# Optimization experiments

Measured on AMD Instinct MI355X. Metric: run time of the kernel, lower is better.

Reference implementation:

```python
import jax, jax.numpy as jnp
import numpy as np

E = 512
H = 8
SL = (16, 16, 16)
B = 4
LEN = np.array([768, 640, 704, 600], dtype=np.int32)


def _starts(lengths):
    cs = jnp.cumsum(lengths)
    starts = jnp.concatenate([jnp.zeros((1,), cs.dtype), cs[:-1]])
    return starts, cs


def _tile_within(data, lengths, buffer):
    # per-token causal window [cur, cur-1, ..., cur-L]; slots before sample start come from buffer
    L = buffer.shape[0]
    N = data.shape[0]
    starts, cs = _starts(lengths)
    g = jnp.arange(N)
    sid = jnp.searchsorted(cs, g, side='right')
    qpos = g - starts[sid]
    src = qpos[:, None] - jnp.arange(L + 1)[None, :]  # [N, L+1]
    from_data = src >= 0
    didx = jnp.clip(starts[sid][:, None] + src, 0, N - 1)
    bidx = jnp.clip(L + src, 0, L - 1)
    return jnp.where(from_data[:, :, None], data[didx], buffer[bidx])


def _mlp(h, w1, b1, w2, b2):
    return jax.nn.gelu(h @ w1 + b1, approximate=False) @ w2 + b2


def _selection(eu, lengths, win):
    # faithful port of the no_grad selection block (B > 1 branch)
    N = eu.shape[0]
    starts, _ = _starts(lengths)
    ends = starts + lengths - 1
    running = jnp.cumsum(eu)
    end_u = running[ends]
    sample_u = jnp.concatenate([end_u[:1], end_u[2:] - end_u[1:-1]])
    running = running - jnp.cumsum(jnp.zeros((N,), eu.dtype).at[starts[1:]].set(sample_u))
    offs = jnp.cumsum(jnp.zeros((N,), eu.dtype).at[starts[1:]].set(lengths[:-1].astype(eu.dtype)))
    idxs = jnp.arange(1, N + 1, dtype=eu.dtype) - offs
    selected = (eu > running / idxs) | (idxs <= win)
    csel = jnp.cumsum(selected.astype(jnp.int32))
    end_counts = csel[ends]
    next_lengths = jnp.concatenate([end_counts[:1], end_counts[1:] - end_counts[:-1]])
    take_map = csel - csel[0]  # unique_consecutive inverse of a 0/1-increment cumsum
    return jnp.nonzero(selected)[0], next_lengths, take_map


def _forward(args, lengths, sels):
    (x, kv_w, kv_b, q_w, q_b, proj_w, proj_b, buf0, buf1, buf2,
     d0_w1, d0_b1, d0_w2, d0_b2, d1_w1, d1_b1, d1_w2, d1_b2,
     u0_w1, u0_b1, u0_w2, u0_b2, u1_w1, u1_b1, u1_w2, u1_b2,
     wq, bq, wk, bk, wv, bv, out_w, out_b) = args
    Ls = [int(v) for v in np.asarray(lengths)]
    x_flat = jnp.concatenate([x[b, :Ls[b]] for b in range(len(Ls))])  # [N0, E]
    kv0 = x_flat @ kv_w + kv_b  # [N0, 2E]
    # scale 0
    tiled0 = _tile_within(kv0, lengths, buf0)  # [N0, SL0, 2E]
    eu0 = jax.nn.elu(_mlp(tiled0.reshape(tiled0.shape[0], -1), u0_w1, u0_b1, u0_w2, u0_b2))[:, 0] + 1.0
    s0 = _selection(jax.lax.stop_gradient(eu0), lengths, SL[0]) if sels is None else sels[0]
    sel0, len1, tm0 = s0
    selt0 = jnp.take(tiled0, sel0, 0)
    r0 = jax.nn.softmax(_mlp(selt0.reshape(selt0.shape[0], -1), d0_w1, d0_b1, d0_w2, d0_b2), -1)
    dat1 = jnp.sum(selt0 * r0[:, :, None], -2)  # [N1, 2E]
    util0 = _tile_within(jnp.take(eu0, sel0, 0)[:, None], len1, jnp.zeros((SL[1] - 1, 1), eu0.dtype))
    # scale 1
    tiled1 = _tile_within(dat1, len1, buf1)  # [N1, SL1, 2E]
    eu1 = jax.nn.elu(_mlp(tiled1.reshape(tiled1.shape[0], -1), u1_w1, u1_b1, u1_w2, u1_b2))[:, 0] + 1.0
    s1 = _selection(jax.lax.stop_gradient(eu1), len1, SL[1]) if sels is None else sels[1]
    sel1, len2, tm1 = s1
    selt1 = jnp.take(tiled1, sel1, 0)
    r1 = jax.nn.softmax(_mlp(selt1.reshape(selt1.shape[0], -1), d1_w1, d1_b1, d1_w2, d1_b2), -1)
    dat2 = jnp.sum(selt1 * r1[:, :, None], -2)  # [N2, 2E]
    util1 = _tile_within(jnp.take(eu1, sel1, 0)[:, None], len2, jnp.zeros((SL[2] - 1, 1), eu1.dtype))
    tiled2 = _tile_within(dat2, len2, buf2)  # [N2, SL2, 2E]
    # per-token multi-scale kv context (reconstructed tail of truncated forward)
    idx1 = tm0
    idx2 = jnp.take(tm1, idx1)
    win1 = jnp.take(tiled1, idx1, 0) * jnp.take(util0, idx1, 0)
    win2 = jnp.take(tiled2, idx2, 0) * jnp.take(util1, idx2, 0)
    kv = jnp.concatenate([tiled0, win1, win2], 1)  # [N0, sum(SL), 2E]
    k = kv[..., :E]
    v = kv[..., E:]
    q = x_flat @ q_w + q_b
    N0 = q.shape[0]
    Skv = kv.shape[1]
    hd = E // H
    qh = (q @ wq + bq).reshape(N0, H, hd)
    kh = (k @ wk + bk).reshape(N0, Skv, H, hd)
    vh = (v @ wv + bv).reshape(N0, Skv, H, hd)
    attn = jax.nn.softmax(jnp.einsum('nhd,nshd->nhs', qh, kh) / float(np.sqrt(hd)), -1)
    ctx = jnp.einsum('nhs,nshd->nhd', attn, vh).reshape(N0, E)
    y = (ctx @ out_w + out_b) @ proj_w + proj_b  # dropout in eval mode == identity
    out = jnp.zeros((len(Ls), max(Ls), E), y.dtype)
    off = 0
    for b, Lb in enumerate(Ls):
        out = out.at[b, :Lb].set(y[off:off + Lb])
        off += Lb
    return out, (s0, s1)


def setup_inputs():
    ks = list(jax.random.split(jax.random.key(0), 64))
    it = iter(ks)

    def nrm(shape, s=0.02):
        return jax.random.normal(next(it), shape, jnp.float32) * s

    def uni(shape):
        return jax.random.uniform(next(it), shape, dtype=jnp.float32)

    F = 2 * E
    inp = {
        'x': jax.random.normal(next(it), (B, int(LEN.max()), E), jnp.float32),
        'lengths': jnp.array(LEN),
        'kv_w': nrm((E, F)), 'kv_b': jnp.zeros((F,), jnp.float32),
        'q_w': nrm((E, E)), 'q_b': jnp.zeros((E,), jnp.float32),
        'proj_w': nrm((E, E)), 'proj_b': jnp.zeros((E,), jnp.float32),
        'buf0': uni((SL[0] - 1, F)), 'buf1': uni((SL[1] - 1, F)), 'buf2': uni((SL[2] - 1, F)),
    }
    for li in (0, 1):
        sl = SL[li]
        din, hid = sl * F, sl * 10
        inp['d%d_w1' % li] = nrm((din, hid)); inp['d%d_b1' % li] = jnp.zeros((hid,), jnp.float32)
        inp['d%d_w2' % li] = nrm((hid, sl)); inp['d%d_b2' % li] = jnp.zeros((sl,), jnp.float32)
        inp['u%d_w1' % li] = nrm((din, hid)); inp['u%d_b1' % li] = jnp.zeros((hid,), jnp.float32)
        inp['u%d_w2' % li] = nrm((hid, 1)); inp['u%d_b2' % li] = jnp.zeros((1,), jnp.float32)
    inp.update({'wq': nrm((E, E)), 'bq': jnp.zeros((E,), jnp.float32),
                'wk': nrm((E, E)), 'bk': jnp.zeros((E,), jnp.float32),
                'wv': nrm((E, E)), 'bv': jnp.zeros((E,), jnp.float32),
                'out_w': nrm((E, E)), 'out_b': jnp.zeros((E,), jnp.float32)})
    return inp


def reference(x, lengths, kv_w, kv_b, q_w, q_b, proj_w, proj_b, buf0, buf1, buf2,
              d0_w1, d0_b1, d0_w2, d0_b2, d1_w1, d1_b1, d1_w2, d1_b2,
              u0_w1, u0_b1, u0_w2, u0_b2, u1_w1, u1_b1, u1_w2, u1_b2,
              wq, bq, wk, bk, wv, bv, out_w, out_b):
    args = (x, kv_w, kv_b, q_w, q_b, proj_w, proj_b, buf0, buf1, buf2,
            d0_w1, d0_b1, d0_w2, d0_b2, d1_w1, d1_b1, d1_w2, d1_b2,
            u0_w1, u0_b1, u0_w2, u0_b2, u1_w1, u1_b1, u1_w2, u1_b2,
            wq, bq, wk, bk, wv, bv, out_w, out_b)
    out, _ = _forward(args, lengths, None)
    return out
```

## Files before the change

### kernel.cpp

```cpp
#include <hip/hip_runtime.h>
#include <cstddef>

#define DEVFN __device__ __forceinline__

constexpr int N0   = 2712;
constexpr int MAXL = 768;
constexpr int NBAT = 4;
constexpr int E    = 512;
constexpr int F    = 1024;
constexpr int HID  = 160;
constexpr int WSZ  = 16;
constexpr int NY   = 2 * WSZ * HID;
constexpr int XSTR = 7680;
constexpr int YC0  = 2560;
constexpr size_t NOFF = (size_t)-1;

constexpr size_t oXF    = 0;
constexpr size_t oXO    = oXF    + (size_t)N0*E;
constexpr size_t oEU0   = oXO    + (size_t)N0*XSTR;
constexpr size_t oDAT1  = oEU0   + (size_t)N0;
constexpr size_t oEU1   = oDAT1  + (size_t)N0*F;
constexpr size_t oDAT2  = oEU1   + (size_t)N0;
constexpr size_t oBH0K  = oDAT2  + (size_t)N0*F;
constexpr size_t oBH0V  = oBH0K  + (size_t)15*E;
constexpr size_t oDH1K  = oBH0V  + (size_t)15*E;
constexpr size_t oDH1V  = oDH1K  + (size_t)N0*E;
constexpr size_t oDH2K  = oDH1V  + (size_t)N0*E;
constexpr size_t oDH2V  = oDH2K  + (size_t)N0*E;
constexpr size_t oCTX   = oDH2V  + (size_t)N0*E;
constexpr size_t oY2    = oCTX   + (size_t)N0*E;
constexpr size_t oEUS0  = oY2    + (size_t)N0*E;
constexpr size_t oEUS1  = oEUS0  + (size_t)N0;
constexpr size_t oSEL0  = oEUS1  + (size_t)N0;
constexpr size_t oTM0   = oSEL0  + (size_t)N0;
constexpr size_t oSEL1  = oTM0   + (size_t)N0;
constexpr size_t oTM1   = oSEL1  + (size_t)N0;
constexpr size_t oB0    = oTM1   + (size_t)N0;
constexpr size_t oB1    = oB0    + 8;
constexpr size_t oB2    = oB1    + 8;
constexpr size_t oWOP   = oB2    + 8;
constexpr size_t oBOP   = oWOP   + (size_t)E*E;
constexpr size_t oWX    = oBOP   + E;
constexpr size_t oXB    = oWX    + (size_t)E*XSTR;
constexpr size_t oBD0   = oXB    + XSTR;
constexpr size_t oBD1   = oBD0   + (size_t)F*NY;
constexpr size_t oBUFY0 = oBD1   + (size_t)F*NY;
constexpr size_t oBUFY1 = oBUFY0 + (size_t)15*NY;
constexpr size_t oYB    = oBUFY1 + (size_t)15*NY;
constexpr size_t oEND   = oYB    + (size_t)N0*NY;

__device__ float g_pool[oEND];

DEVFN float geluf(float x) {
    return 0.5f * x * (1.0f + erff(x / 1.41421356237309504880f));
}

__global__ void k_init() {
    if (threadIdx.x == 0) {
        int* b = (int*)(g_pool + oB0);
        b[0] = 0; b[1] = 768; b[2] = 1408; b[3] = 2112; b[4] = N0;
    }
}

__global__ __launch_bounds__(256) void k_xflat(const float* __restrict__ x) {
    int idx = blockIdx.x * 256 + threadIdx.x;
    if (idx >= N0 * E) return;
    int d = idx & (E - 1);
    int g = idx >> 9;
    int s = (g >= 768) + (g >= 1408) + (g >= 2112);
    const int st[4] = {0, 768, 1408, 2112};
    int qp = g - st[s];
    g_pool[oXF + idx] = x[((size_t)s * MAXL + qp) * E + d];
}

__global__ __launch_bounds__(256) void k_reshape(
    const float* __restrict__ uw, const float* __restrict__ dw, size_t bdOff)
{
    int idx = blockIdx.x * 256 + threadIdx.x;
    if (idx >= F * NY) return;
    int col = idx % NY;
    int f = idx / NY;
    const float* src = (col < NY / 2) ? uw : dw;
    int rem = (col < NY / 2) ? col : col - NY / 2;
    int j = rem / HID, n = rem % HID;
    g_pool[bdOff + idx] = src[((size_t)j * F + f) * HID + n];
}

__global__ __launch_bounds__(256) void k_copymat(
    const float* __restrict__ src, size_t dstOff, int rows, int cols, int lds, int ldd)
{
    int idx = blockIdx.x * 256 + threadIdx.x;
    if (idx >= rows * cols) return;
    int r = idx / cols, c = idx % cols;
    g_pool[dstOff + (size_t)r * ldd + c] = src[(size_t)r * lds + c];
}

__global__ __launch_bounds__(256) void k_prepvec(
    const float* __restrict__ kv_b, const float* __restrict__ q_b, const float* __restrict__ out_b,
    const float* __restrict__ wk, const float* __restrict__ bk,
    const float* __restrict__ wv, const float* __restrict__ bv,
    const float* __restrict__ wq, const float* __restrict__ bq,
    const float* __restrict__ proj_w, const float* __restrict__ proj_b)
{
    int idx = blockIdx.x * 256 + threadIdx.x;
    if (idx >= 3072) return;
    if (idx < 1024) { g_pool[oXB + idx] = kv_b[idx]; return; }
    const float* vec; const float* W; const float* add; int n; size_t dst;
    if (idx < 1536)      { n = idx - 1024; vec = kv_b;     W = wk;     add = bk;     dst = oXB + idx; }
    else if (idx < 2048) { n = idx - 1536; vec = kv_b + E; W = wv;     add = bv;     dst = oXB + idx; }
    else if (idx < 2560) { n = idx - 2048; vec = q_b;      W = wq;     add = bq;     dst = oXB + idx; }
    else                 { n = idx - 2560; vec = out_b;    W = proj_w; add = proj_b; dst = oBOP + n; }
    float s = add[n];
    for (int k = 0; k < E; ++k) s = fmaf(vec[k], W[(size_t)k * E + n], s);
    g_pool[dst] = s;
}

__global__ __launch_bounds__(256) void k_cvec(const float* __restrict__ kv_b) {
    int n = blockIdx.x * 256 + threadIdx.x;
    if (n >= NY) return;
    const float* BD = g_pool + oBD0;
    float s = 0.0f;
    for (int k = 0; k < F; ++k) s = fmaf(kv_b[k], BD[(size_t)k * NY + n], s);
    g_pool[oXB + YC0 + n] = s;
}

DEVFN void gemm64_body(
    const float* __restrict__ A, int lda,
    const float* __restrict__ B, int ldb,
    const float* __restrict__ bias,
    float* __restrict__ C, int ldc,
    int mval, int row0, int col0, int K, int N)
{
    __shared__ __align__(16) float As[32][68];
    __shared__ __align__(16) float Bs[32][64];

    int tid = threadIdx.x;
    float acc[4][4] = {};
    int tx = tid & 15, ty = tid >> 4;

    for (int k0 = 0; k0 < K; k0 += 32) {
        #pragma unroll
        for (int l = 0; l < 8; ++l) {
            int idx = tid + l * 256;
            int kk = idx & 31, m = idx >> 5;
            int r = row0 + m;
            float v = 0.0f;
            if (r < mval) v = A[(size_t)r * lda + k0 + kk];
            As[kk][m] = v;
        }
        #pragma unroll
        for (int l = 0; l < 8; ++l) {
            int idx = tid + l * 256;
            int n = idx & 63, kk = idx >> 6;
            int col = col0 + n;
            float v = 0.0f;
            if (col < N) v = B[(size_t)(k0 + kk) * ldb + col];
            Bs[kk][n] = v;
        }
        __syncthreads();
        #pragma unroll
        for (int kk = 0; kk < 32; ++kk) {
            float4 a4 = *(const float4*)&As[kk][ty * 4];
            float4 b4 = *(const float4*)&Bs[kk][tx * 4];
            float av[4] = {a4.x, a4.y, a4.z, a4.w};
            float bv[4] = {b4.x, b4.y, b4.z, b4.w};
            #pragma unroll
            for (int i = 0; i < 4; ++i)
                #pragma unroll
                for (int jn = 0; jn < 4; ++jn)
                    acc[i][jn] = fmaf(av[i], bv[jn], acc[i][jn]);
        }
        __syncthreads();
    }

    #pragma unroll
    for (int i = 0; i < 4; ++i) {
        int r = row0 + ty * 4 + i;
        if (r >= mval) continue;
        #pragma unroll
        for (int jn = 0; jn < 4; ++jn) {
            int col = col0 + tx * 4 + jn;
            if (col < N)
                C[(size_t)r * ldc + col] = acc[i][jn] + (bias ? bias[col] : 0.0f);
        }
    }
}

__global__ __launch_bounds__(256) void k_pgemm(
    size_t Aoff, int lda, size_t Boff, int ldb, size_t biasOff,
    size_t Coff, int ldc, int M, size_t mdevOff, int K, int N)
{
    int mval = (mdevOff == NOFF) ? M : *(const int*)(g_pool + mdevOff);
    int row0 = blockIdx.x * 64, col0 = blockIdx.y * 64;
    if (row0 >= mval) return;
    gemm64_body(g_pool + Aoff, lda, g_pool + Boff, ldb,
                (biasOff == NOFF) ? nullptr : g_pool + biasOff,
                g_pool + Coff, ldc, mval, row0, col0, K, N);
}

__global__ __launch_bounds__(256) void k_wprep(
    const float* __restrict__ kv_w, const float* __restrict__ q_w, const float* __restrict__ out_w,
    const float* __restrict__ wk, const float* __restrict__ wv,
    const float* __restrict__ wq, const float* __restrict__ proj_w)
{
    int z = blockIdx.z;
    const float* A; int lda; const float* B; float* C; int ldc;
    if (z == 0)      { A = kv_w;     lda = F; B = wk;     C = g_pool + oWX + 1024; ldc = XSTR; }
    else if (z == 1) { A = kv_w + E; lda = F; B = wv;     C = g_pool + oWX + 1536; ldc = XSTR; }
    else if (z == 2) { A = q_w;      lda = E; B = wq;     C = g_pool + oWX + 2048; ldc = XSTR; }
    else             { A = out_w;    lda = E; B = proj_w; C = g_pool + oWOP;       ldc = E;    }
    gemm64_body(A, lda, B, E, nullptr, C, ldc, E, blockIdx.x * 64, blockIdx.y * 64, E, E);
}

__global__ __launch_bounds__(256) void k_bufy(
    const float* __restrict__ buf0, const float* __restrict__ buf1)
{
    int z = blockIdx.z;
    const float* A = z ? buf1 : buf0;
    const float* B = g_pool + (z ? oBD1 : oBD0);
    float* C = g_pool + (z ? oBUFY1 : oBUFY0);
    gemm64_body(A, F, B, NY, nullptr, C, NY, 15, 0, blockIdx.y * 64, F, NY);
}

__global__ __launch_bounds__(256) void k_bh(
    const float* __restrict__ buf0,
    const float* __restrict__ wk, const float* __restrict__ bk,
    const float* __restrict__ wv, const float* __restrict__ bv)
{
    int z = blockIdx.z;
    const float* A = buf0 + (size_t)z * E;
    const float* B = z ? wv : wk;
    const float* bias = z ? bv : bk;
    float* C = g_pool + (z ? oBH0V : oBH0K);
    gemm64_body(A, F, B, E, bias, C, E, 15, 0, blockIdx.y * 64, E, E);
}

DEVFN void fma_8x8(const float4& a0, const float4& a1, const float4& b0, const float4& b1,
                   float2 (&acc)[8][4])
{
    float av[8] = {a0.x, a0.y, a0.z, a0.w, a1.x, a1.y, a1.z, a1.w};
    float2 bv[4] = {make_float2(b0.x, b0.y), make_float2(b0.z, b0.w),
                    make_float2(b1.x, b1.y), make_float2(b1.z, b1.w)};
    #pragma unroll
    for (int i = 0; i < 8; ++i) {
        #pragma unroll
        for (int q = 0; q < 4; ++q) {
            acc[i][q].x = fmaf(av[i], bv[q].x, acc[i][q].x);
            acc[i][q].y = fmaf(av[i], bv[q].y, acc[i][q].y);
        }
    }
}

DEVFN void gemm128_body(
    const float* __restrict__ A, int lda,
    const float* __restrict__ B, int ldb,
    const float* __restrict__ bias,
    float* __restrict__ C, int ldc,
    int mval, int row0, int col0, int K)
{
    __shared__ __align__(16) float As[16][132];
    __shared__ __align__(16) float Bs[16][132];

    int tid = threadIdx.x;
    int tx = tid & 15, ty = tid >> 4;
    float2 acc[8][4] = {};

    int ar = tid >> 1, akq = (tid & 1) * 8;
    int bk = tid >> 4, bnq = (tid & 15) * 8;

    for (int k0 = 0; k0 < K; k0 += 16) {
        {
            float4 v0 = make_float4(0.f, 0.f, 0.f, 0.f), v1 = v0;
            int rr = row0 + ar;
            if (rr < mval) {
                v0 = *(const float4*)&A[(size_t)rr * lda + k0 + akq];
                v1 = *(const float4*)&A[(size_t)rr * lda + k0 + akq + 4];
            }
            As[akq + 0][ar] = v0.x; As[akq + 1][ar] = v0.y;
            As[akq + 2][ar] = v0.z; As[akq + 3][ar] = v0.w;
            As[akq + 4][ar] = v1.x; As[akq + 5][ar] = v1.y;
            As[akq + 6][ar] = v1.z; As[akq + 7][ar] = v1.w;
        }
        {
            const float* bp = &B[(size_t)(k0 + bk) * ldb + col0 + bnq];
            *(float4*)&Bs[bk][bnq]     = *(const float4*)&bp[0];
            *(float4*)&Bs[bk][bnq + 4] = *(const float4*)&bp[4];
        }
        __syncthreads();

        float4 a0A = *(const float4*)&As[0][ty * 8];
        float4 a1A = *(const float4*)&As[0][ty * 8 + 4];
        float4 b0A = *(const float4*)&Bs[0][tx * 4];
        float4 b1A = *(const float4*)&Bs[0][64 + tx * 4];
        #pragma unroll
        for (int kk = 0; kk < 16; kk += 2) {
            float4 a0B = *(const float4*)&As[kk + 1][ty * 8];
            float4 a1B = *(const float4*)&As[kk + 1][ty * 8 + 4];
            float4 b0B = *(const float4*)&Bs[kk + 1][tx * 4];
            float4 b1B = *(const float4*)&Bs[kk + 1][64 + tx * 4];
            fma_8x8(a0A, a1A, b0A, b1A, acc);
            if (kk + 2 < 16) {
                a0A = *(const float4*)&As[kk + 2][ty * 8];
                a1A = *(const float4*)&As[kk + 2][ty * 8 + 4];
                b0A = *(const float4*)&Bs[kk + 2][tx * 4];
                b1A = *(const float4*)&Bs[kk + 2][64 + tx * 4];
            }
            fma_8x8(a0B, a1B, b0B, b1B, acc);
        }
        __syncthreads();
    }

    #pragma unroll
    for (int i = 0; i < 8; ++i) {
        int r = row0 + ty * 8 + i;
        if (r >= mval) continue;
        float o0[4], o1[4];
        o0[0] = acc[i][0].x; o0[1] = acc[i][0].y; o0[2] = acc[i][1].x; o0[3] = acc[i][1].y;
        o1[0] = acc[i][2].x; o1[1] = acc[i][2].y; o1[2] = acc[i][3].x; o1[3] = acc[i][3].y;
        if (bias) {
            #pragma unroll
            for (int jn = 0; jn < 4; ++jn) {
                o0[jn] += bias[col0 + tx * 4 + jn];
                o1[jn] += bias[col0 + 64 + tx * 4 + jn];
            }
        }
        *(float4*)&C[(size_t)r * ldc + col0 + tx * 4]      = *(float4*)&o0[0];
        *(float4*)&C[(size_t)r * ldc + col0 + 64 + tx * 4] = *(float4*)&o1[0];
    }
}

__global__ __launch_bounds__(256) void k_tgemm(
    size_t Aoff, int lda, size_t Boff, int ldb, size_t biasOff,
    size_t Coff, int ldc, int M, size_t mdevOff, int K)
{
    int mval = (mdevOff == NOFF) ? M : *(const int*)(g_pool + mdevOff);
    int row0 = blockIdx.x * 128, col0 = blockIdx.y * 128;
    if (row0 >= mval) return;
    gemm128_body(g_pool + Aoff, lda, g_pool + Boff, ldb,
                 (biasOff == NOFF) ? nullptr : g_pool + biasOff,
                 g_pool + Coff, ldc, mval, row0, col0, K);
}

__global__ __launch_bounds__(256) void k_wy(const float* __restrict__ kv_w) {
    int z = blockIdx.z;
    const float* A = kv_w + z * 256;
    const float* B = g_pool + oBD0 + (size_t)z * 256 * NY;
    float* C = g_pool + oYB + (size_t)z * E * NY;
    gemm128_body(A, F, B, NY, nullptr, C, NY, E, blockIdx.x * 128, blockIdx.y * 128, 256);
}

__global__ __launch_bounds__(256) void k_wyred() {
    int idx = blockIdx.x * 256 + threadIdx.x;
    if (idx >= E * NY) return;
    int r = idx / NY, c = idx % NY;
    const float* p = g_pool + oYB;
    float s = ((p[idx] + p[(size_t)E * NY + idx]) + p[(size_t)2 * E * NY + idx]) + p[(size_t)3 * E * NY + idx];
    g_pool[oWX + (size_t)r * XSTR + YC0 + c] = s;
}

__global__ __launch_bounds__(256) void k_zgemm(
    const float* __restrict__ wk, const float* __restrict__ wv)
{
    int z = blockIdx.z;
    int mval = *(const int*)(g_pool + ((z < 2) ? (oB1 + 4) : (oB2 + 4)));
    int row0 = blockIdx.x * 64, col0 = blockIdx.y * 64;
    if (row0 >= mval) return;
    const float* A = g_pool + ((z < 2) ? oDAT1 : oDAT2) + (size_t)(z & 1) * E;
    const float* B = (z & 1) ? wv : wk;
    float* C = g_pool + oDH1K + (size_t)z * N0 * E;
    gemm64_body(A, F, B, E, nullptr, C, E, mval, row0, col0, E, E);
}

__global__ void k_huev(
    size_t boundsOff, size_t yOff, int yStr, size_t bufYOff,
    const float* __restrict__ b1, const float* __restrict__ w2, const float* __restrict__ b2,
    size_t euOff, size_t mdevOff, int M)
{
    int i = blockIdx.x;
    int mval = (mdevOff == NOFF) ? M : *(const int*)(g_pool + mdevOff);
    if (i >= mval) return;
    int n = threadIdx.x;

    __shared__ float t[HID];
    const int* bounds = (const int*)(g_pool + boundsOff);
    int b1i = bounds[1], b2i = bounds[2], b3i = bounds[3];
    int s = (i >= b1i) + (i >= b2i) + (i >= b3i);
    int st = (s == 0) ? 0 : ((s == 1) ? b1i : ((s == 2) ? b2i : b3i));
    int qp = i - st;

    const float* Y = g_pool + yOff;
    const float* bufY = g_pool + bufYOff;

    if (n < HID) {
        float acc = b1[n];
        #pragma unroll
        for (int j = 0; j < WSZ; ++j) {
            int sp = qp - j;
            const float* row = (sp >= 0) ? &Y[(size_t)(i - j) * yStr]
                                         : &bufY[(size_t)(15 + sp) * NY];
            acc += row[j * HID + n];
        }
        t[n] = geluf(acc) * w2[n];
    }
    __syncthreads();
    if (n == 0) {
        float v = b2[0];
        for (int k = 0; k < HID; ++k) v += t[k];
        v = (v > 0.0f) ? v : expm1f(v);
        g_pool[euOff + i] = v + 1.0f;
    }
}

__global__ __launch_bounds__(256) void k_select(
    size_t euOff, size_t boundsOff, int win,
    size_t selOff, size_t tmOff, size_t euSelOff, size_t boundsNextOff)
{
    __shared__ __align__(16) float se[N0];
    __shared__ __align__(16) float run[N0];
    __shared__ int sFlag[N0];
    __shared__ int sSum[256];
    __shared__ float sCz[NBAT];
    __shared__ int sEc[NBAT];
    __shared__ int sB[5];

    int tid = threadIdx.x;
    const int* bounds = (const int*)(g_pool + boundsOff);
    if (tid < 5) sB[tid] = bounds[tid];
    __syncthreads();
    int N = sB[4];
    for (int i = tid; i < N; i += 256) se[i] = g_pool[euOff + i];
    __syncthreads();

    if (tid == 0) {
        float r = 0.0f;
        int g = 0;
        for (; g + 8 <= N; g += 8) {
            float4 a = *(const float4*)&se[g];
            float4 b4 = *(const float4*)&se[g + 4];
            r += a.x;  run[g]     = r;
            r += a.y;  run[g + 1] = r;
            r += a.z;  run[g + 2] = r;
            r += a.w;  run[g + 3] = r;
            r += b4.x; run[g + 4] = r;
            r += b4.y; run[g + 5] = r;
            r += b4.z; run[g + 6] = r;
            r += b4.w; run[g + 7] = r;
        }
        for (; g < N; ++g) { r += se[g]; run[g] = r; }
        float e0 = run[sB[1] - 1], e1 = run[sB[2] - 1], e2 = run[sB[3] - 1];
        float su0 = e0;
        float su1 = e2 - e1;
        float su2 = run[sB[4] - 1] - e2;
        sCz[0] = 0.0f;
        sCz[1] = su0;
        sCz[2] = su0 + su1;
        sCz[3] = (su0 + su1) + su2;
    }
    __syncthreads();

    for (int g = tid; g < N; g += 256) {
        int seg = (g >= sB[1]) + (g >= sB[2]) + (g >= sB[3]);
        int st = (seg == 0) ? 0 : sB[seg];
        int qp1 = g - st + 1;
        float r2 = run[g] - sCz[seg];
        bool seld = (se[g] > r2 / (float)qp1) || (qp1 <= win);
        sFlag[g] = seld ? 1 : 0;
    }
    __syncthreads();

    int CH = (N + 255) >> 8;
    int lo = tid * CH, hi = min(lo + CH, N);
    {
        int s = 0;
        for (int g = lo; g < hi; ++g) s += sFlag[g];
        sSum[tid] = s;
    }
    __syncthreads();
    if (tid == 0) {
        int acc = 0;
        for (int t = 0; t < 256; ++t) { int v = sSum[t]; sSum[t] = acc; acc += v; }
    }
    __syncthreads();

    int* sel = (int*)(g_pool + selOff);
    int* tm  = (int*)(g_pool + tmOff);
    float* eus = g_pool + euSelOff;
    int* bn  = (int*)(g_pool + boundsNextOff);

    int csel0 = sFlag[0];
    {
        int csel = sSum[tid];
        for (int g = lo; g < hi; ++g) {
            csel += sFlag[g];
            tm[g] = csel - csel0;
            if (sFlag[g]) { sel[csel - 1] = g; eus[csel - 1] = se[g]; }
            #pragma unroll
            for (int s = 0; s < NBAT; ++s)
                if (g == sB[s + 1] - 1) sEc[s] = csel;
        }
    }
    __syncthreads();
    if (tid == 0) {
        bn[0] = 0; bn[1] = sEc[0]; bn[2] = sEc[1]; bn[3] = sEc[2]; bn[4] = sEc[3];
    }
}

__global__ __launch_bounds__(256) void k_rdat(
    size_t boundsOff, size_t yOff, int yStr, size_t bufYOff,
    const float* __restrict__ b1, const float* __restrict__ w2, const float* __restrict__ b2,
    size_t selOff, size_t mdevOff,
    size_t srcOff, int srcStr, const float* __restrict__ buf,
    size_t datOff)
{
    int i = blockIdx.x;
    if (i >= *(const int*)(g_pool + mdevOff)) return;
    const float* src = g_pool + srcOff;
    const int* bounds = (const int*)(g_pool + boundsOff);
    const int* sel = (const int*)(g_pool + selOff);
    float* dat = g_pool + datOff;

    __shared__ float gh[HID];
    __shared__ float sv[WSZ];
    __shared__ float r[WSZ];
    __shared__ int sG, sQp;

    int tid = threadIdx.x;
    if (tid == 0) {
        int g = sel[i];
        int b1i = bounds[1], b2i = bounds[2], b3i = bounds[3];
        int s = (g >= b1i) + (g >= b2i) + (g >= b3i);
        int st = (s == 0) ? 0 : ((s == 1) ? b1i : ((s == 2) ? b2i : b3i));
        sG = g; sQp = g - st;
    }
    __syncthreads();
    int g = sG, qp = sQp;

    if (tid < HID) {
        const float* Y = g_pool + yOff;
        const float* bufY = g_pool + bufYOff;
        float acc = b1[tid];
        #pragma unroll
        for (int j = 0; j < WSZ; ++j) {
            int sp = qp - j;
            const float* row = (sp >= 0) ? &Y[(size_t)(g - j) * yStr]
                                         : &bufY[(size_t)(15 + sp) * NY];
            acc += row[NY / 2 + j * HID + tid];
        }
        gh[tid] = geluf(acc);
    }
    __syncthreads();
    if (tid < WSZ) {
        float acc = 0.0f;
        for (int k = 0; k < HID; ++k) acc += gh[k] * w2[k * WSZ + tid];
        sv[tid] = acc + b2[tid];
    }
    __syncthreads();
    if (tid == 0) {
        float m = sv[0];
        for (int t = 1; t < WSZ; ++t) m = fmaxf(m, sv[t]);
        float sum = 0.0f;
        for (int t = 0; t < WSZ; ++t) { float e = expf(sv[t] - m); r[t] = e; sum += e; }
        for (int t = 0; t < WSZ; ++t) r[t] = r[t] / sum;
    }
    __syncthreads();
    for (int f = tid; f < F; f += 256) {
        float acc = 0.0f;
        for (int j = 0; j < WSZ; ++j) {
            int sp = qp - j;
            float v = (sp >= 0) ? src[(size_t)(g - j) * srcStr + f]
                                : buf[(size_t)(15 + sp) * F + f];
            acc = fmaf(r[j], v, acc);
        }
        dat[(size_t)i * F + f] = acc;
    }
}

__global__ __launch_bounds__(512) void k_attn(
    const float* __restrict__ bk, const float* __restrict__ bv)
{
    int g = blockIdx.x;
    const float* XO   = g_pool + oXO;
    const float* BH0k = g_pool + oBH0K;
    const float* BH0v = g_pool + oBH0V;
    const float* DH1k = g_pool + oDH1K;
    const float* DH1v = g_pool + oDH1V;
    const float* DH2k = g_pool + oDH2K;
    const float* DH2v = g_pool + oDH2V;
    const float* eus0 = g_pool + oEUS0;
    const float* eus1 = g_pool + oEUS1;
    const int* tm0 = (const int*)(g_pool + oTM0);
    const int* tm1 = (const int*)(g_pool + oTM1);
    const int* bounds1 = (const int*)(g_pool + oB1);
    const int* bounds2 = (const int*)(g_pool + oB2);

    __shared__ const float* sK[48];
    __shared__ const float* sV[48];
    __shared__ float sScale[48];
    __shared__ __align__(16) float sQ[E], sBk[E], sBv[E];
    __shared__ float sc[48][8];

    int tid = threadIdx.x;
    sQ[tid]  = XO[(size_t)g * XSTR + 2048 + tid];
    sBk[tid] = bk[tid];
    sBv[tid] = bv[tid];

    if (tid < 48) {
        int s = tid;
        const float *pK = nullptr, *pV = nullptr;
        float scl = 0.0f;
        if (s < 16) {
            int s0 = (g >= 768) + (g >= 1408) + (g >= 2112);
            const int st0[4] = {0, 768, 1408, 2112};
            int sp = (g - st0[s0]) - s;
            if (sp >= 0) { pK = XO + (size_t)(g - s) * XSTR + 1024; pV = XO + (size_t)(g - s) * XSTR + 1536; }
            else         { pK = BH0k + (size_t)(15 + sp) * E; pV = BH0v + (size_t)(15 + sp) * E; }
            scl = 1.0f;
        } else if (s < 32) {
            int j = s - 16;
            int i1 = tm0[g];
            int b1 = bounds1[1], b2 = bounds1[2], b3 = bounds1[3];
            int sg = (i1 >= b1) + (i1 >= b2) + (i1 >= b3);
            int st = (sg == 0) ? 0 : ((sg == 1) ? b1 : ((sg == 2) ? b2 : b3));
            int sp = (i1 - st) - j;
            if (sp >= 0) { pK = DH1k + (size_t)(i1 - j) * E; pV = DH1v + (size_t)(i1 - j) * E; scl = eus0[i1 - j]; }
        } else {
            int j = s - 32;
            int i1 = tm0[g];
            int i2 = tm1[i1];
            int b1 = bounds2[1], b2 = bounds2[2], b3 = bounds2[3];
            int sg = (i2 >= b1) + (i2 >= b2) + (i2 >= b3);
            int st = (sg == 0) ? 0 : ((sg == 1) ? b1 : ((sg == 2) ? b2 : b3));
            int sp = (i2 - st) - j;
            if (sp >= 0) { pK = DH2k + (size_t)(i2 - j) * E; pV = DH2v + (size_t)(i2 - j) * E; scl = eus1[i2 - j]; }
        }
        sK[s] = pK; sV[s] = pV; sScale[s] = scl;
    }
    __syncthreads();

    if (tid < 384) {
        int s = tid >> 3, h = tid & 7;
        const float* bp = sK[s];
        float scl = sScale[s];
        float acc = 0.0f;
        int d0 = h * 64;
        if (s < 16) {
            for (int d = 0; d < 64; d += 4) {
                float4 qv = *(const float4*)&sQ[d0 + d];
                float4 kv4 = *(const float4*)&bp[d0 + d];
                acc += qv.x * kv4.x; acc += qv.y * kv4.y;
                acc += qv.z * kv4.z; acc += qv.w * kv4.w;
            }
        } else if (bp) {
            for (int d = 0; d < 64; d += 4) {
                float4 qv = *(const float4*)&sQ[d0 + d];
                float4 kv4 = *(const float4*)&bp[d0 + d];
                float4 bb = *(const float4*)&sBk[d0 + d];
                acc += qv.x * (bb.x + scl * kv4.x); acc += qv.y * (bb.y + scl * kv4.y);
                acc += qv.z * (bb.z + scl * kv4.z); acc += qv.w * (bb.w + scl * kv4.w);
            }
        } else {
            for (int d = 0; d < 64; d += 4) {
                float4 qv = *(const float4*)&sQ[d0 + d];
                float4 bb = *(const float4*)&sBk[d0 + d];
                acc += qv.x * bb.x; acc += qv.y * bb.y;
                acc += qv.z * bb.z; acc += qv.w * bb.w;
            }
        }
        sc[s][h] = acc * 0.125f;
    }
    __syncthreads();

    if (tid < 8) {
        int h = tid;
        float m = sc[0][h];
        for (int s = 1; s < 48; ++s) m = fmaxf(m, sc[s][h]);
        float sum = 0.0f;
        for (int s = 0; s < 48; ++s) { float e = expf(sc[s][h] - m); sc[s][h] = e; sum += e; }
        for (int s = 0; s < 48; ++s) sc[s][h] = sc[s][h] / sum;
    }
    __syncthreads();

    {
        int d = tid, h = d >> 6;
        float acc = 0.0f;
        for (int s = 0; s < 48; ++s) {
            const float* bp = sV[s];
            float vv;
            if (s < 16) vv = bp[d];
            else        vv = sBv[d] + (bp ? sScale[s] * bp[d] : 0.0f);
            acc = fmaf(sc[s][h], vv, acc);
        }
        g_pool[oCTX + (size_t)g * E + d] = acc;
    }
}

__global__ __launch_bounds__(256) void k_scatter(float* __restrict__ out) {
    int idx = blockIdx.x * 256 + threadIdx.x;
    if (idx >= NBAT * MAXL * E) return;
    int d = idx & (E - 1);
    int rest = idx >> 9;
    int p = rest % MAXL, bb = rest / MAXL;
    const int st[4] = {0, 768, 1408, 2112};
    const int ln[4] = {768, 640, 704, 600};
    out[idx] = (p < ln[bb]) ? g_pool[oY2 + (size_t)(st[bb] + p) * E + d] : 0.0f;
}

extern "C" void kernel_launch(void* const* d_in, const int* in_sizes, int n_in,
                              void* d_out, int out_size, void* d_ws, size_t ws_size,
                              hipStream_t stream)
{
    (void)in_sizes; (void)n_in; (void)d_ws; (void)ws_size; (void)out_size;

    const float* x      = (const float*)d_in[0];
    const float* kv_w   = (const float*)d_in[2];
    const float* kv_b   = (const float*)d_in[3];
    const float* q_w    = (const float*)d_in[4];
    const float* q_b    = (const float*)d_in[5];
    const float* proj_w = (const float*)d_in[6];
    const float* proj_b = (const float*)d_in[7];
    const float* buf0   = (const float*)d_in[8];
    const float* buf1   = (const float*)d_in[9];
    const float* d0_w1  = (const float*)d_in[11];
    const float* d0_b1  = (const float*)d_in[12];
    const float* d0_w2  = (const float*)d_in[13];
    const float* d0_b2  = (const float*)d_in[14];
    const float* u0_w1  = (const float*)d_in[15];
    const float* u0_b1  = (const float*)d_in[16];
    const float* u0_w2  = (const float*)d_in[17];
    const float* u0_b2  = (const float*)d_in[18];
    const float* d1_w1  = (const float*)d_in[19];
    const float* d1_b1  = (const float*)d_in[20];
    const float* d1_w2  = (const float*)d_in[21];
    const float* d1_b2  = (const float*)d_in[22];
    const float* u1_w1  = (const float*)d_in[23];
    const float* u1_b1  = (const float*)d_in[24];
    const float* u1_w2  = (const float*)d_in[25];
    const float* u1_b2  = (const float*)d_in[26];
    const float* wq     = (const float*)d_in[27];
    const float* bq     = (const float*)d_in[28];
    const float* wk     = (const float*)d_in[29];
    const float* bk     = (const float*)d_in[30];
    const float* wv     = (const float*)d_in[31];
    const float* bv     = (const float*)d_in[32];
    const float* out_w  = (const float*)d_in[33];
    const float* out_b  = (const float*)d_in[34];

    auto cdiv = [](int a, int b) { return (a + b - 1) / b; };
    auto GT = [&](int M, int N) { return dim3(cdiv(M, 128), cdiv(N, 128)); };

    k_init<<<1, 64, 0, stream>>>();
    k_xflat<<<cdiv(N0 * E, 256), 256, 0, stream>>>(x);

    k_reshape<<<cdiv(F * NY, 256), 256, 0, stream>>>(u0_w1, d0_w1, oBD0);
    k_reshape<<<cdiv(F * NY, 256), 256, 0, stream>>>(u1_w1, d1_w1, oBD1);
    k_copymat<<<cdiv(E * F, 256), 256, 0, stream>>>(kv_w, oWX, E, F, F, XSTR);
    k_wprep<<<dim3(8, 8, 4), 256, 0, stream>>>(kv_w, q_w, out_w, wk, wv, wq, proj_w);
    k_prepvec<<<cdiv(3072, 256), 256, 0, stream>>>(kv_b, q_b, out_b, wk, bk, wv, bv, wq, bq, proj_w, proj_b);
    k_cvec<<<cdiv(NY, 256), 256, 0, stream>>>(kv_b);
    k_wy<<<dim3(4, 40, 4), 256, 0, stream>>>(kv_w);
    k_wyred<<<cdiv(E * NY, 256), 256, 0, stream>>>();
    k_bufy<<<dim3(1, NY / 64, 2), 256, 0, stream>>>(buf0, buf1);
    k_bh<<<dim3(1, E / 64, 2), 256, 0, stream>>>(buf0, wk, bk, wv, bv);

    k_tgemm<<<GT(N0, XSTR), 256, 0, stream>>>(oXF, E, oWX, XSTR, oXB, oXO, XSTR, N0, NOFF, E);

    k_huev<<<N0, 160, 0, stream>>>(oB0, oXO + YC0, XSTR, oBUFY0, u0_b1, u0_w2, u0_b2, oEU0, NOFF, N0);
    k_select<<<1, 256, 0, stream>>>(oEU0, oB0, WSZ, oSEL0, oTM0, oEUS0, oB1);
    k_rdat<<<N0, 256, 0, stream>>>(oB0, oXO + YC0, XSTR, oBUFY0, d0_b1, d0_w2, d0_b2, oSEL0, oB1 + 4, oXO, XSTR, buf0, oDAT1);

    k_tgemm<<<GT(N0, NY), 256, 0, stream>>>(oDAT1, F, oBD1, NY, NOFF, oYB, NY, N0, oB1 + 4, F);
    k_huev<<<N0, 160, 0, stream>>>(oB1, oYB, NY, oBUFY1, u1_b1, u1_w2, u1_b2, oEU1, oB1 + 4, N0);
    k_select<<<1, 256, 0, stream>>>(oEU1, oB1, WSZ, oSEL1, oTM1, oEUS1, oB2);
    k_rdat<<<N0, 256, 0, stream>>>(oB1, oYB, NY, oBUFY1, d1_b1, d1_w2, d1_b2, oSEL1, oB2 + 4, oDAT1, F, buf1, oDAT2);

    k_zgemm<<<dim3(cdiv(N0, 64), E / 64, 4), 256, 0, stream>>>(wk, wv);

    k_attn<<<N0, 512, 0, stream>>>(bk, bv);
    k_pgemm<<<dim3(cdiv(N0, 64), E / 64), 256, 0, stream>>>(oCTX, E, oWOP, E, oBOP, oY2, E, N0, NOFF, E, E);
    k_scatter<<<cdiv(NBAT * MAXL * E, 256), 256, 0, stream>>>((float*)d_out);
}
```

Measured before the change: 1.380 ms.

## Fold scale-1 K/V projections into the level-1 GEMM and vectorise rdat accumulation

Extends the level-1 weight matrix with block-diagonal wk/wv columns (zero-padded halves), so the scale-1 K/V projections come out of the existing DAT1 GEMM instead of a separate zgemm pass. The zgemm launch shrinks to the scale-2 K and V only, and attention reads scale-1 K/V directly from the widened YB buffer. Separately, k_rdat now has each thread accumulate four contiguous features with float4 loads. The fused GEMM multiplies against zero blocks, wasting about half its FLOPs on the new columns, and the assumption F==4*256 is baked into rdat.

```diff
diff --git a/kernel.cpp b/kernel.cpp
--- a/kernel.cpp
+++ b/kernel.cpp
@@ -11,6 +11,9 @@
 constexpr int HID  = 160;
 constexpr int WSZ  = 16;
 constexpr int NY   = 2 * WSZ * HID;
+constexpr int NY1  = 6144;
+constexpr int DH1KC = 5120;
+constexpr int DH1VC = 5632;
 constexpr int XSTR = 7680;
 constexpr int YC0  = 2560;
 constexpr size_t NOFF = (size_t)-1;
@@ -23,9 +26,7 @@
 constexpr size_t oDAT2  = oEU1   + (size_t)N0;
 constexpr size_t oBH0K  = oDAT2  + (size_t)N0*F;
 constexpr size_t oBH0V  = oBH0K  + (size_t)15*E;
-constexpr size_t oDH1K  = oBH0V  + (size_t)15*E;
-constexpr size_t oDH1V  = oDH1K  + (size_t)N0*E;
-constexpr size_t oDH2K  = oDH1V  + (size_t)N0*E;
+constexpr size_t oDH2K  = oBH0V  + (size_t)15*E;
 constexpr size_t oDH2V  = oDH2K  + (size_t)N0*E;
 constexpr size_t oCTX   = oDH2V  + (size_t)N0*E;
 constexpr size_t oY2    = oCTX   + (size_t)N0*E;
@@ -44,10 +45,10 @@
 constexpr size_t oXB    = oWX    + (size_t)E*XSTR;
 constexpr size_t oBD0   = oXB    + XSTR;
 constexpr size_t oBD1   = oBD0   + (size_t)F*NY;
-constexpr size_t oBUFY0 = oBD1   + (size_t)F*NY;
+constexpr size_t oBUFY0 = oBD1   + (size_t)F*NY1;
 constexpr size_t oBUFY1 = oBUFY0 + (size_t)15*NY;
 constexpr size_t oYB    = oBUFY1 + (size_t)15*NY;
-constexpr size_t oEND   = oYB    + (size_t)N0*NY;
+constexpr size_t oEND   = oYB    + (size_t)N0*NY1;
 
 __device__ float g_pool[oEND];
 
@@ -84,6 +85,30 @@
     int rem = (col < NY / 2) ? col : col - NY / 2;
     int j = rem / HID, n = rem % HID;
     g_pool[bdOff + idx] = src[((size_t)j * F + f) * HID + n];
+}
+
+__global__ __launch_bounds__(256) void k_bd1x(
+    const float* __restrict__ uw, const float* __restrict__ dw,
+    const float* __restrict__ wk, const float* __restrict__ wv)
+{
+    int idx = blockIdx.x * 256 + threadIdx.x;
+    if (idx >= F * NY1) return;
+    int col = idx % NY1;
+    int f = idx / NY1;
+    float v;
+    if (col < NY) {
+        const float* src = (col < NY / 2) ? uw : dw;
+        int rem = (col < NY / 2) ? col : col - NY / 2;
+        int j = rem / HID, n = rem % HID;
+        v = src[((size_t)j * F + f) * HID + n];
+    } else if (col < DH1VC) {
+        int m = col - DH1KC;
+        v = (f < E) ? wk[(size_t)f * E + m] : 0.0f;
+    } else {
+        int m = col - DH1VC;
+        v = (f >= E) ? wv[(size_t)(f - E) * E + m] : 0.0f;
+    }
+    g_pool[oBD1 + idx] = v;
 }
 
 __global__ __launch_bounds__(256) void k_copymat(
@@ -218,8 +243,9 @@
     int z = blockIdx.z;
     const float* A = z ? buf1 : buf0;
     const float* B = g_pool + (z ? oBD1 : oBD0);
+    int ldb = z ? NY1 : NY;
     float* C = g_pool + (z ? oBUFY1 : oBUFY0);
-    gemm64_body(A, F, B, NY, nullptr, C, NY, 15, 0, blockIdx.y * 64, F, NY);
+    gemm64_body(A, F, B, ldb, nullptr, C, NY, 15, 0, blockIdx.y * 64, F, NY);
 }
 
 __global__ __launch_bounds__(256) void k_bh(
@@ -362,12 +388,12 @@
     const float* __restrict__ wk, const float* __restrict__ wv)
 {
     int z = blockIdx.z;
-    int mval = *(const int*)(g_pool + ((z < 2) ? (oB1 + 4) : (oB2 + 4)));
+    int mval = *(const int*)(g_pool + oB2 + 4);
     int row0 = blockIdx.x * 64, col0 = blockIdx.y * 64;
     if (row0 >= mval) return;
-    const float* A = g_pool + ((z < 2) ? oDAT1 : oDAT2) + (size_t)(z & 1) * E;
-    const float* B = (z & 1) ? wv : wk;
-    float* C = g_pool + oDH1K + (size_t)z * N0 * E;
+    const float* A = g_pool + oDAT2 + (size_t)z * E;
+    const float* B = z ? wv : wk;
+    float* C = g_pool + (z ? oDH2V : oDH2K);
     gemm64_body(A, F, B, E, nullptr, C, E, mval, row0, col0, E, E);
 }
 
@@ -563,15 +589,22 @@
         for (int t = 0; t < WSZ; ++t) r[t] = r[t] / sum;
     }
     __syncthreads();
-    for (int f = tid; f < F; f += 256) {
-        float acc = 0.0f;
+    {
+        int f0 = tid * 4;
+        float4 acc = make_float4(0.f, 0.f, 0.f, 0.f);
+        #pragma unroll
         for (int j = 0; j < WSZ; ++j) {
             int sp = qp - j;
-            float v = (sp >= 0) ? src[(size_t)(g - j) * srcStr + f]
-                                : buf[(size_t)(15 + sp) * F + f];
-            acc = fmaf(r[j], v, acc);
-        }
-        dat[(size_t)i * F + f] = acc;
+            const float* row = (sp >= 0) ? &src[(size_t)(g - j) * srcStr]
+                                         : &buf[(size_t)(15 + sp) * F];
+            float4 v = *(const float4*)&row[f0];
+            float rj = r[j];
+            acc.x = fmaf(rj, v.x, acc.x);
+            acc.y = fmaf(rj, v.y, acc.y);
+            acc.z = fmaf(rj, v.z, acc.z);
+            acc.w = fmaf(rj, v.w, acc.w);
+        }
+        *(float4*)&dat[(size_t)i * F + f0] = acc;
     }
 }
 
@@ -582,8 +615,7 @@
     const float* XO   = g_pool + oXO;
     const float* BH0k = g_pool + oBH0K;
     const float* BH0v = g_pool + oBH0V;
-    const float* DH1k = g_pool + oDH1K;
-    const float* DH1v = g_pool + oDH1V;
+    const float* Y1X  = g_pool + oYB;
     const float* DH2k = g_pool + oDH2K;
     const float* DH2v = g_pool + oDH2V;
     const float* eus0 = g_pool + oEUS0;
@@ -622,7 +654,11 @@
             int sg = (i1 >= b1) + (i1 >= b2) + (i1 >= b3);
             int st = (sg == 0) ? 0 : ((sg == 1) ? b1 : ((sg == 2) ? b2 : b3));
             int sp = (i1 - st) - j;
-            if (sp >= 0) { pK = DH1k + (size_t)(i1 - j) * E; pV = DH1v + (size_t)(i1 - j) * E; scl = eus0[i1 - j]; }
+            if (sp >= 0) {
+                pK = Y1X + (size_t)(i1 - j) * NY1 + DH1KC;
+                pV = Y1X + (size_t)(i1 - j) * NY1 + DH1VC;
+                scl = eus0[i1 - j];
+            }
         } else {
             int j = s - 32;
             int i1 = tm0[g];
@@ -752,7 +788,7 @@
     k_xflat<<<cdiv(N0 * E, 256), 256, 0, stream>>>(x);
 
     k_reshape<<<cdiv(F * NY, 256), 256, 0, stream>>>(u0_w1, d0_w1, oBD0);
-    k_reshape<<<cdiv(F * NY, 256), 256, 0, stream>>>(u1_w1, d1_w1, oBD1);
+    k_bd1x<<<cdiv(F * NY1, 256), 256, 0, stream>>>(u1_w1, d1_w1, wk, wv);
     k_copymat<<<cdiv(E * F, 256), 256, 0, stream>>>(kv_w, oWX, E, F, F, XSTR);
     k_wprep<<<dim3(8, 8, 4), 256, 0, stream>>>(kv_w, q_w, out_w, wk, wv, wq, proj_w);
     k_prepvec<<<cdiv(3072, 256), 256, 0, stream>>>(kv_b, q_b, out_b, wk, bk, wv, bv, wq, bq, proj_w, proj_b);
@@ -768,12 +804,12 @@
     k_select<<<1, 256, 0, stream>>>(oEU0, oB0, WSZ, oSEL0, oTM0, oEUS0, oB1);
     k_rdat<<<N0, 256, 0, stream>>>(oB0, oXO + YC0, XSTR, oBUFY0, d0_b1, d0_w2, d0_b2, oSEL0, oB1 + 4, oXO, XSTR, buf0, oDAT1);
 
-    k_tgemm<<<GT(N0, NY), 256, 0, stream>>>(oDAT1, F, oBD1, NY, NOFF, oYB, NY, N0, oB1 + 4, F);
-    k_huev<<<N0, 160, 0, stream>>>(oB1, oYB, NY, oBUFY1, u1_b1, u1_w2, u1_b2, oEU1, oB1 + 4, N0);
+    k_tgemm<<<GT(N0, NY1), 256, 0, stream>>>(oDAT1, F, oBD1, NY1, NOFF, oYB, NY1, N0, oB1 + 4, F);
+    k_huev<<<N0, 160, 0, stream>>>(oB1, oYB, NY1, oBUFY1, u1_b1, u1_w2, u1_b2, oEU1, oB1 + 4, N0);
     k_select<<<1, 256, 0, stream>>>(oEU1, oB1, WSZ, oSEL1, oTM1, oEUS1, oB2);
-    k_rdat<<<N0, 256, 0, stream>>>(oB1, oYB, NY, oBUFY1, d1_b1, d1_w2, d1_b2, oSEL1, oB2 + 4, oDAT1, F, buf1, oDAT2);
-
-    k_zgemm<<<dim3(cdiv(N0, 64), E / 64, 4), 256, 0, stream>>>(wk, wv);
+    k_rdat<<<N0, 256, 0, stream>>>(oB1, oYB, NY1, oBUFY1, d1_b1, d1_w2, d1_b2, oSEL1, oB2 + 4, oDAT1, F, buf1, oDAT2);
+
+    k_zgemm<<<dim3(cdiv(N0, 64), E / 64, 2), 256, 0, stream>>>(wk, wv);
 
     k_attn<<<N0, 512, 0, stream>>>(bk, bv);
     k_pgemm<<<dim3(cdiv(N0, 64), E / 64), 256, 0, stream>>>(oCTX, E, oWOP, E, oBOP, oY2, E, N0, NOFF, E, E);
```

Result: no change. 1.363 ms (-1.2%).
